# Kernel tuning notes

Hardware: AMD Instinct MI355X
Metric: run time of the kernel (lower is better)

## Reference

```python
import jax, jax.numpy as jnp
import numpy as np

B, T, D, HS = 8, 2048, 1024, 64  # batch, seq, num_embd, head_size


def setup_inputs() -> dict:
    key = jax.random.key(0)
    kc, kq, kk, kv = jax.random.split(key, 4)
    return {
        "context": jax.random.normal(kc, (B, T, D), dtype=jnp.float32),
        "Wq": jax.random.normal(kq, (D, HS), dtype=jnp.float32) * (D ** -0.5),
        "Wk": jax.random.normal(kk, (D, HS), dtype=jnp.float32) * (D ** -0.5),
        "Wv": jax.random.normal(kv, (D, HS), dtype=jnp.float32) * (D ** -0.5),
    }


def reference(context, Wq, Wk, Wv):
    # context: [B, T, D]; projections: [B, T, HS]
    q = context @ Wq
    k = context @ Wk
    v = context @ Wv
    scale = k.shape[-1] ** -0.5
    # scores: [B, T, T], causal mask, stable softmax (dropout p=0 -> identity)
    wei = jnp.einsum("btd,bsd->bts", q, k) * scale
    t = wei.shape[-1]
    causal = jnp.tril(jnp.ones((t, t), dtype=bool))
    wei = jnp.where(causal, wei, -jnp.inf)
    wei = jax.nn.softmax(wei, axis=-1)
    return jnp.einsum("bts,bsh->bth", wei, v)
```

## Files before the change

### kernel.cpp

```cpp
#include <hip/hip_runtime.h>
#include <math.h>

#define BB 8
#define TT 2048
#define DD 1024
#define HSZ 64

typedef __bf16 bf16_t;
typedef bf16_t bf16x8 __attribute__((ext_vector_type(8)));
typedef bf16_t bf16x4 __attribute__((ext_vector_type(4)));
typedef float f32x4 __attribute__((ext_vector_type(4)));

#define MFMA16(A, B, C) __builtin_amdgcn_mfma_f32_16x16x32_bf16(A, B, C, 0, 0, 0)


__global__ __launch_bounds__(256) void wt_convert(
    const float* __restrict__ Wq, const float* __restrict__ Wk,
    const float* __restrict__ Wv, bf16_t* __restrict__ Wtf)
{
    int id = blockIdx.x * 256 + threadIdx.x;
    int j = id & 7;
    int lane = (id >> 3) & 63;
    int chunk = (id >> 9) & 31;
    int nt = id >> 14;
    int l16 = lane & 15, quad = lane >> 4;
    int k = chunk * 32 + quad * 8 + j;
    int col = nt * 16 + l16;
    int m = col >> 6, ncol = col & 63;
    const float* W = (m == 0) ? Wq : (m == 1) ? Wk : Wv;
    float scl = (m == 0) ? 0.18033688f : 1.0f;
    Wtf[id] = (bf16_t)(W[k * HSZ + ncol] * scl);
}

__global__ __launch_bounds__(256) void qkv_proj(
    const float* __restrict__ ctx, const bf16_t* __restrict__ Wtf,
    bf16_t* __restrict__ Q, bf16_t* __restrict__ Kf, bf16_t* __restrict__ Vf)
{
    __shared__ __align__(16) char smem_raw[32 * 1032 * 2];
    bf16_t (*As)[1032] = (bf16_t (*)[1032])smem_raw;
    f32x4 (*red)[4][4][64] = (f32x4 (*)[4][4][64])smem_raw;

    const int tid = threadIdx.x;
    const int w = tid >> 6, lane = tid & 63;
    const int quad = lane >> 4, l16 = lane & 15;
    const size_t row0 = (size_t)blockIdx.x * 32;
    const int k0 = w * 256;

    {
        const float4* csrc = (const float4*)(ctx + row0 * DD);
        #pragma unroll
        for (int i = 0; i < 32; ++i) {
            float4 v = csrc[i * 256 + tid];
            bf16x4 bv;
            bv[0] = (bf16_t)v.x; bv[1] = (bf16_t)v.y;
            bv[2] = (bf16_t)v.z; bv[3] = (bf16_t)v.w;
            *(bf16x4*)&As[i][tid * 4] = bv;
        }
    }
    __syncthreads();

    f32x4 acc0[12], acc1[12];
    #pragma unroll
    for (int i = 0; i < 12; ++i) {
        acc0[i] = (f32x4){0.f, 0.f, 0.f, 0.f};
        acc1[i] = (f32x4){0.f, 0.f, 0.f, 0.f};
    }

    const bf16_t* wbase = Wtf + lane * 8;

    #pragma unroll
    for (int kc = 0; kc < 256; kc += 32) {
        const int chunk = (k0 + kc) >> 5;
        bf16x8 af0 = *(const bf16x8*)&As[l16][k0 + kc + quad * 8];
        bf16x8 af1 = *(const bf16x8*)&As[16 + l16][k0 + kc + quad * 8];
        #pragma unroll
        for (int nt = 0; nt < 12; ++nt) {
            bf16x8 bfr = *(const bf16x8*)(wbase + ((size_t)nt * 32 + chunk) * 512);
            acc0[nt] = MFMA16(af0, bfr, acc0[nt]);
            acc1[nt] = MFMA16(af1, bfr, acc1[nt]);
        }
    }
    __syncthreads();

    const int bb   = (int)(row0 >> 11);
    const int tloc = (int)(row0 & 2047);
    const int kt   = tloc >> 6;

    #pragma unroll
    for (int r = 0; r < 3; ++r) {
        if (r) __syncthreads();
        #pragma unroll
        for (int i = 0; i < 4; ++i) {
            red[0][w][i][lane] = acc0[r * 4 + i];
            red[1][w][i][lane] = acc1[r * 4 + i];
        }
        __syncthreads();

        #pragma unroll
        for (int m = 0; m < 2; ++m) {
            f32x4 s = red[m][0][w][lane];
            s += red[m][1][w][lane];
            s += red[m][2][w][lane];
            s += red[m][3][w][lane];

            const int tm = tloc + m * 16;

            if (r == 0) {
                const int col = w * 16 + l16;
                #pragma unroll
                for (int reg = 0; reg < 4; ++reg)
                    Q[(row0 + m * 16 + quad * 4 + reg) * HSZ + col] = (bf16_t)s[reg];
            } else if (r == 1) {
                const int nn = (tm >> 4) & 3;
                const int ks = w >> 1;
                const int quadf = (w & 1) * 2 + (l16 >> 3);
                const int jj = l16 & 7;
                const size_t fb = ((((size_t)bb * 32 + kt) * 4 + nn) * 2 + ks) * 512;
                #pragma unroll
                for (int reg = 0; reg < 4; ++reg)
                    Kf[fb + (quadf * 16 + quad * 4 + reg) * 8 + jj] = (bf16_t)s[reg];
            } else {
                const int t0 = tm + quad * 4;
                const int ks = (t0 >> 5) & 1;
                const int quadf = (t0 >> 3) & 3;
                const int j0 = t0 & 7;
                const size_t fb = ((((size_t)bb * 32 + kt) * 2 + ks) * 4 + w) * 512;
                bf16x4 v;
                #pragma unroll
                for (int reg = 0; reg < 4; ++reg) v[reg] = (bf16_t)s[reg];
                *(bf16x4*)(Vf + fb + (quadf * 16 + l16) * 8 + j0) = v;
            }
        }
    }
}

__device__ __forceinline__ void load_kfrags(
    const bf16_t* __restrict__ Kf, size_t bofs, int kt, int lane, bf16x8* kf)
{
    const bf16_t* kbase = Kf + ((bofs + (size_t)kt) * 8) * 512 + lane * 8;
    #pragma unroll
    for (int i = 0; i < 8; ++i)
        kf[i] = *(const bf16x8*)(kbase + i * 512);
}

#define WREG 8704

__global__ __launch_bounds__(256, 2) void attn_kernel(
    const bf16_t* __restrict__ Q, const bf16_t* __restrict__ Kf,
    const bf16_t* __restrict__ Vf, float* __restrict__ O)
{
    __shared__ __align__(16) char sm[4 * WREG + 512];

    const int tid = threadIdx.x;
    const int w = tid >> 6, lane = tid & 63;
    const int quad = lane >> 4, l16 = lane & 15;

    bf16_t (*Psw)[72] = (bf16_t (*)[72])(sm + w * WREG);
    float  (*Orw)[68] = (float  (*)[68])(sm + w * WREG);
    float* Lred = (float*)(sm + 4 * WREG);

    const int z = blockIdx.x;
    const int b = z & 7;
    const int s = z >> 3;
    const int js = (s < 32) ? (63 - s) : (s - 32);
    const size_t base = (size_t)b * TT * HSZ;
    const size_t bofs = (size_t)b * 32;
    const int ntile = (js >> 1) + 1;
    const int q0 = js << 5;

    bf16x8 qf0[2], qf1[2];
    #pragma unroll
    for (int g = 0; g < 2; ++g) {
        const bf16_t* qp = Q + base + (size_t)(q0 + g * 16 + l16) * HSZ + quad * 8;
        qf0[g] = *(const bf16x8*)qp;
        qf1[g] = *(const bf16x8*)(qp + 32);
    }

    bf16x8 onesA;
    #pragma unroll
    for (int i = 0; i < 8; ++i) onesA[i] = (bf16_t)1.0f;

    f32x4 o[2][4];
    f32x4 lacc[2];
    #pragma unroll
    for (int g = 0; g < 2; ++g) {
        #pragma unroll
        for (int dt = 0; dt < 4; ++dt) o[g][dt] = (f32x4){0.f, 0.f, 0.f, 0.f};
        lacc[g] = (f32x4){0.f, 0.f, 0.f, 0.f};
    }

    bf16x8 kA[8], kB[8];

    auto process = [&](int kt, const bf16x8* kf) {
        const bool last = (kt == ntile - 1);

        const bf16_t* vbase = Vf + ((bofs + (size_t)kt) * 8) * 512 + lane * 8;
        bf16x8 vf[8];
        #pragma unroll
        for (int i = 0; i < 8; ++i)
            vf[i] = *(const bf16x8*)(vbase + i * 512);

        #pragma unroll
        for (int g = 0; g < 2; ++g) {
            const int jmg = (2 * js + g) & 3;
            const int nv = last ? jmg + 1 : 4;

            f32x4 sc[4];
            #pragma unroll
            for (int n = 0; n < 4; ++n) {
                if (n < nv) {
                    f32x4 a = (f32x4){0.f, 0.f, 0.f, 0.f};
                    a = MFMA16(kf[2 * n], qf0[g], a);
                    a = MFMA16(kf[2 * n + 1], qf1[g], a);
                    sc[n] = a;
                }
            }

            if (last) {
                #pragma unroll
                for (int n = 0; n < 4; ++n) {
                    if (n < nv) {
                        #pragma unroll
                        for (int reg = 0; reg < 4; ++reg) {
                            bool masked = (n == jmg) && (quad * 4 + reg > l16);
                            float p = __builtin_amdgcn_exp2f(sc[n][reg]);
                            sc[n][reg] = masked ? 0.f : p;
                        }
                    }
                }
            } else {
                #pragma unroll
                for (int n = 0; n < 4; ++n)
                    #pragma unroll
                    for (int reg = 0; reg < 4; ++reg)
                        sc[n][reg] = __builtin_amdgcn_exp2f(sc[n][reg]);
            }

            #pragma unroll
            for (int n = 0; n < 4; ++n) {
                bf16x4 pv;
                #pragma unroll
                for (int reg = 0; reg < 4; ++reg)
                    pv[reg] = (bf16_t)((n < nv) ? sc[n][reg] : 0.f);
                *(bf16x4*)&Psw[g * 16 + l16][n * 16 + quad * 4] = pv;
            }
        }

        #pragma unroll
        for (int g = 0; g < 2; ++g) {
            const int nv = last ? ((2 * js + g) & 3) + 1 : 4;
            const int ksm = (nv > 2) ? 2 : 1;
            bf16x8 pf0 = *(const bf16x8*)&Psw[g * 16 + l16][quad * 8];
            bf16x8 pf1 = *(const bf16x8*)&Psw[g * 16 + l16][32 + quad * 8];
            #pragma unroll
            for (int dt = 0; dt < 4; ++dt) {
                o[g][dt] = MFMA16(vf[dt], pf0, o[g][dt]);
                if (ksm == 2) o[g][dt] = MFMA16(vf[4 + dt], pf1, o[g][dt]);
            }
            lacc[g] = MFMA16(onesA, pf0, lacc[g]);
            if (ksm == 2) lacc[g] = MFMA16(onesA, pf1, lacc[g]);
        }
    };

    if (w < ntile) {
        load_kfrags(Kf, bofs, w, lane, kA);
        for (int kt = w; kt < ntile; kt += 8) {
            if (kt + 4 < ntile) load_kfrags(Kf, bofs, kt + 4, lane, kB);
            process(kt, kA);
            if (kt + 4 < ntile) {
                if (kt + 8 < ntile) load_kfrags(Kf, bofs, kt + 8, lane, kA);
                process(kt + 4, kB);
            }
        }
    }

    #pragma unroll
    for (int g = 0; g < 2; ++g) {
        #pragma unroll
        for (int dt = 0; dt < 4; ++dt)
            *(f32x4*)&Orw[g * 16 + l16][dt * 16 + quad * 4] = o[g][dt];
        if (quad == 0) Lred[w * 32 + g * 16 + l16] = lacc[g][0];
    }
    __syncthreads();

    #pragma unroll
    for (int rep = 0; rep < 2; ++rep) {
        const int idx = rep * 256 + tid;
        const int query = idx >> 4, d4 = idx & 15;
        float l = Lred[0 * 32 + query] + Lred[1 * 32 + query] +
                  Lred[2 * 32 + query] + Lred[3 * 32 + query];
        f32x4 sv = *(const f32x4*)((const float*)(sm + 0 * WREG) + query * 68 + d4 * 4);
        sv += *(const f32x4*)((const float*)(sm + 1 * WREG) + query * 68 + d4 * 4);
        sv += *(const f32x4*)((const float*)(sm + 2 * WREG) + query * 68 + d4 * 4);
        sv += *(const f32x4*)((const float*)(sm + 3 * WREG) + query * 68 + d4 * 4);
        const float linv = 1.f / l;
        float4 outv = make_float4(sv[0] * linv, sv[1] * linv,
                                  sv[2] * linv, sv[3] * linv);
        *(float4*)(O + base + (size_t)(q0 + query) * HSZ + d4 * 4) = outv;
    }
}

extern "C" void kernel_launch(void* const* d_in, const int* in_sizes, int n_in,
                              void* d_out, int out_size, void* d_ws, size_t ws_size,
                              hipStream_t stream) {
    const float* ctx = (const float*)d_in[0];
    const float* Wq  = (const float*)d_in[1];
    const float* Wk  = (const float*)d_in[2];
    const float* Wv  = (const float*)d_in[3];
    float* out = (float*)d_out;

    const size_t NQ = (size_t)BB * TT * HSZ;
    bf16_t* Qw  = (bf16_t*)d_ws;
    bf16_t* Kfw = Qw + NQ;
    bf16_t* Vfw = Kfw + NQ;
    bf16_t* Wtf = Vfw + NQ;

    wt_convert<<<768, 256, 0, stream>>>(Wq, Wk, Wv, Wtf);
    qkv_proj<<<512, 256, 0, stream>>>(ctx, Wtf, Qw, Kfw, Vfw);
    attn_kernel<<<512, 256, 0, stream>>>(Qw, Kfw, Vfw, out);
}
```

Before: 121.7 us.

## Split QKV projection by output columns per wave, removing split-K reduction

The projection kernel now processes 16 rows per block instead of 32, launching twice as many blocks. Each wave computes full-K dot products for its own 16-column slice of Q, K and V, instead of splitting K across waves and reducing through shared memory. This removes the shared-memory reduction and its barriers, cuts LDS use, and allows four blocks per CU. In exchange, weight fragments are reused across fewer rows and the per-wave MFMA chains are longer and serial.

```diff
diff --git a/kernel.cpp b/kernel.cpp
--- a/kernel.cpp
+++ b/kernel.cpp
@@ -32,24 +32,21 @@
     Wtf[id] = (bf16_t)(W[k * HSZ + ncol] * scl);
 }
 
-__global__ __launch_bounds__(256) void qkv_proj(
+__global__ __launch_bounds__(256, 4) void qkv_proj(
     const float* __restrict__ ctx, const bf16_t* __restrict__ Wtf,
     bf16_t* __restrict__ Q, bf16_t* __restrict__ Kf, bf16_t* __restrict__ Vf)
 {
-    __shared__ __align__(16) char smem_raw[32 * 1032 * 2];
-    bf16_t (*As)[1032] = (bf16_t (*)[1032])smem_raw;
-    f32x4 (*red)[4][4][64] = (f32x4 (*)[4][4][64])smem_raw;
+    __shared__ __align__(16) bf16_t As[16][1032];
 
     const int tid = threadIdx.x;
     const int w = tid >> 6, lane = tid & 63;
     const int quad = lane >> 4, l16 = lane & 15;
-    const size_t row0 = (size_t)blockIdx.x * 32;
-    const int k0 = w * 256;
+    const size_t row0 = (size_t)blockIdx.x * 16;
 
     {
         const float4* csrc = (const float4*)(ctx + row0 * DD);
         #pragma unroll
-        for (int i = 0; i < 32; ++i) {
+        for (int i = 0; i < 16; ++i) {
             float4 v = csrc[i * 256 + tid];
             bf16x4 bv;
             bv[0] = (bf16_t)v.x; bv[1] = (bf16_t)v.y;
@@ -59,78 +56,56 @@
     }
     __syncthreads();
 
-    f32x4 acc0[12], acc1[12];
-    #pragma unroll
-    for (int i = 0; i < 12; ++i) {
-        acc0[i] = (f32x4){0.f, 0.f, 0.f, 0.f};
-        acc1[i] = (f32x4){0.f, 0.f, 0.f, 0.f};
-    }
+    f32x4 aq = (f32x4){0.f, 0.f, 0.f, 0.f};
+    f32x4 ak = (f32x4){0.f, 0.f, 0.f, 0.f};
+    f32x4 av = (f32x4){0.f, 0.f, 0.f, 0.f};
 
     const bf16_t* wbase = Wtf + lane * 8;
-
-    #pragma unroll
-    for (int kc = 0; kc < 256; kc += 32) {
-        const int chunk = (k0 + kc) >> 5;
-        bf16x8 af0 = *(const bf16x8*)&As[l16][k0 + kc + quad * 8];
-        bf16x8 af1 = *(const bf16x8*)&As[16 + l16][k0 + kc + quad * 8];
-        #pragma unroll
-        for (int nt = 0; nt < 12; ++nt) {
-            bf16x8 bfr = *(const bf16x8*)(wbase + ((size_t)nt * 32 + chunk) * 512);
-            acc0[nt] = MFMA16(af0, bfr, acc0[nt]);
-            acc1[nt] = MFMA16(af1, bfr, acc1[nt]);
-        }
-    }
-    __syncthreads();
+    const bf16_t* wq = wbase + (size_t)(w)     * 32 * 512;
+    const bf16_t* wk = wbase + (size_t)(4 + w) * 32 * 512;
+    const bf16_t* wv = wbase + (size_t)(8 + w) * 32 * 512;
+
+    #pragma unroll 4
+    for (int chunk = 0; chunk < 32; ++chunk) {
+        bf16x8 af = *(const bf16x8*)&As[l16][chunk * 32 + quad * 8];
+        bf16x8 bq = *(const bf16x8*)(wq + (size_t)chunk * 512);
+        bf16x8 bk = *(const bf16x8*)(wk + (size_t)chunk * 512);
+        bf16x8 bv = *(const bf16x8*)(wv + (size_t)chunk * 512);
+        aq = MFMA16(af, bq, aq);
+        ak = MFMA16(af, bk, ak);
+        av = MFMA16(af, bv, av);
+    }
 
     const int bb   = (int)(row0 >> 11);
     const int tloc = (int)(row0 & 2047);
     const int kt   = tloc >> 6;
 
-    #pragma unroll
-    for (int r = 0; r < 3; ++r) {
-        if (r) __syncthreads();
-        #pragma unroll
-        for (int i = 0; i < 4; ++i) {
-            red[0][w][i][lane] = acc0[r * 4 + i];
-            red[1][w][i][lane] = acc1[r * 4 + i];
-        }
-        __syncthreads();
-
-        #pragma unroll
-        for (int m = 0; m < 2; ++m) {
-            f32x4 s = red[m][0][w][lane];
-            s += red[m][1][w][lane];
-            s += red[m][2][w][lane];
-            s += red[m][3][w][lane];
-
-            const int tm = tloc + m * 16;
-
-            if (r == 0) {
-                const int col = w * 16 + l16;
-                #pragma unroll
-                for (int reg = 0; reg < 4; ++reg)
-                    Q[(row0 + m * 16 + quad * 4 + reg) * HSZ + col] = (bf16_t)s[reg];
-            } else if (r == 1) {
-                const int nn = (tm >> 4) & 3;
-                const int ks = w >> 1;
-                const int quadf = (w & 1) * 2 + (l16 >> 3);
-                const int jj = l16 & 7;
-                const size_t fb = ((((size_t)bb * 32 + kt) * 4 + nn) * 2 + ks) * 512;
-                #pragma unroll
-                for (int reg = 0; reg < 4; ++reg)
-                    Kf[fb + (quadf * 16 + quad * 4 + reg) * 8 + jj] = (bf16_t)s[reg];
-            } else {
-                const int t0 = tm + quad * 4;
-                const int ks = (t0 >> 5) & 1;
-                const int quadf = (t0 >> 3) & 3;
-                const int j0 = t0 & 7;
-                const size_t fb = ((((size_t)bb * 32 + kt) * 2 + ks) * 4 + w) * 512;
-                bf16x4 v;
-                #pragma unroll
-                for (int reg = 0; reg < 4; ++reg) v[reg] = (bf16_t)s[reg];
-                *(bf16x4*)(Vf + fb + (quadf * 16 + l16) * 8 + j0) = v;
-            }
-        }
+    {
+        const int col = w * 16 + l16;
+        #pragma unroll
+        for (int reg = 0; reg < 4; ++reg)
+            Q[(row0 + quad * 4 + reg) * HSZ + col] = (bf16_t)aq[reg];
+    }
+    {
+        const int nn = (tloc >> 4) & 3;
+        const int ks = w >> 1;
+        const int quadf = (w & 1) * 2 + (l16 >> 3);
+        const int jj = l16 & 7;
+        const size_t fb = ((((size_t)bb * 32 + kt) * 4 + nn) * 2 + ks) * 512;
+        #pragma unroll
+        for (int reg = 0; reg < 4; ++reg)
+            Kf[fb + (quadf * 16 + quad * 4 + reg) * 8 + jj] = (bf16_t)ak[reg];
+    }
+    {
+        const int t0 = tloc + quad * 4;
+        const int ks = (t0 >> 5) & 1;
+        const int quadf = (t0 >> 3) & 3;
+        const int j0 = t0 & 7;
+        const size_t fb = ((((size_t)bb * 32 + kt) * 2 + ks) * 4 + w) * 512;
+        bf16x4 v;
+        #pragma unroll
+        for (int reg = 0; reg < 4; ++reg) v[reg] = (bf16_t)av[reg];
+        *(bf16x4*)(Vf + fb + (quadf * 16 + l16) * 8 + j0) = v;
     }
 }
 
@@ -316,6 +291,6 @@
     bf16_t* Wtf = Vfw + NQ;
 
     wt_convert<<<768, 256, 0, stream>>>(Wq, Wk, Wv, Wtf);
-    qkv_proj<<<512, 256, 0, stream>>>(ctx, Wtf, Qw, Kfw, Vfw);
+    qkv_proj<<<1024, 256, 0, stream>>>(ctx, Wtf, Qw, Kfw, Vfw);
     attn_kernel<<<512, 256, 0, stream>>>(Qw, Kfw, Vfw, out);
 }
```

Measured after the change: 120.2 us. No clear change (-1.2%).
